# Performance work log

Measured on AMD Instinct MI355X. Metric: run time of the kernel, lower is better.

Reference implementation:

```python
import jax, jax.numpy as jnp
import numpy as np

FACTOR = 5  # init arg 'factor'


def setup_inputs() -> dict:
    key = jax.random.key(0)
    ks = jax.random.split(key, 9)
    B, L, H, D = 32, 4096, 8, 64
    sh = (B, L, H, D)
    scale = 0.125  # 1/sqrt(D)
    return {
        "queries": jax.random.normal(ks[0], sh, jnp.float32),
        "keys": jax.random.normal(ks[1], sh, jnp.float32),
        "values": jax.random.normal(ks[2], sh, jnp.float32),
        "Wq": jax.random.normal(ks[3], (1, D), jnp.float32) * scale,
        "bq": jax.random.normal(ks[4], (1,), jnp.float32) * scale,
        "Wk": jax.random.normal(ks[5], (1, D), jnp.float32) * scale,
        "bk": jax.random.normal(ks[6], (1,), jnp.float32) * scale,
        "Wv": jax.random.normal(ks[7], (1, D), jnp.float32) * scale,
        "bv": jax.random.normal(ks[8], (1,), jnp.float32) * scale,
    }


def reference(queries, keys, values, Wq, bq, Wk, bk, Wv, bv):
    B, L_Q, H, D = queries.shape
    # transpose(2,1) + LazyLinear(1) + squeeze  ->  scalar series per (b, h, t)
    q = jnp.einsum('blhd,d->bhl', queries, Wq[0]) + bq[0]  # [B,H,L_Q]
    k = jnp.einsum('blhd,d->bhl', keys, Wk[0]) + bk[0]
    v = jnp.einsum('blhd,d->bhl', values, Wv[0]) + bv[0]
    # L_K == L_Q here: torch takes the last L_Q steps (identity in this config)
    k = k[:, :, -L_Q:]
    v = v[:, :, -L_Q:]
    # FFT cross-correlation scores (rfft with n=2L-1 -> L bins; irfft default -> 2L-2)
    n_fft = 2 * L_Q - 1
    Qf = jnp.fft.rfft(q, n_fft)
    Kf = jnp.conj(jnp.fft.rfft(k, n_fft))
    score = jnp.fft.irfft(Qf * Kf)[:, :, :L_Q] / L_Q  # [B,H,L_Q]
    kk = FACTOR * int(np.ceil(np.log(L_Q)))  # 45 for L_Q=4096
    weight, top_idx = jax.lax.top_k(score, kk)  # [B,H,kk]
    weight = jax.nn.softmax(weight, axis=-1)
    # torch: indices = L_Q - top_idx - 1; rolled-V row j is roll(v, j+1),
    # i.e. shift = L_Q - top_idx, so V_sel[b,h,d,t] = v[b,h,(t + top_idx[b,h,d]) % L_Q].
    t = jnp.arange(L_Q)
    gidx = (top_idx[..., None] + t[None, None, None, :]) % L_Q  # [B,H,kk,L_Q]
    V_sel = jnp.take_along_axis(v[:, :, None, :], gidx, axis=-1)  # [B,H,kk,L_Q]
    out = jnp.einsum('bhd,bhdl->bhl', weight, V_sel)  # [B,H,L_Q]
    return out[..., None]  # [B,H,L_Q,1]
```

## Files before the change

kernel.cpp:

```cpp
#include <hip/hip_runtime.h>
#include <math.h>
#include <float.h>

#define L_   4096
#define M_   8192
#define H_   8
#define D_   64
#define KK   45

#define WS_C   0
#define WS_D   4096
#define WS_TW  8192
#define WS_H1  16384
#define WS_H2  24576
#define WS_QKV 32768

typedef unsigned int u32_t;

__device__ __forceinline__ float2 cadd(float2 a, float2 b) { return make_float2(a.x + b.x, a.y + b.y); }
__device__ __forceinline__ float2 csub(float2 a, float2 b) { return make_float2(a.x - b.x, a.y - b.y); }
__device__ __forceinline__ float2 cmulf(float2 a, float2 b) {
  return make_float2(a.x * b.x - a.y * b.y, a.x * b.y + a.y * b.x);
}
__device__ __forceinline__ float2 cmulcf(float2 a, float2 b) {
  return make_float2(a.x * b.x + a.y * b.y, a.y * b.x - a.x * b.y);
}

__device__ __forceinline__ float2 twf(int e) {
  float s, c;
  __sincosf((float)e * -7.66990394e-4f, &s, &c);
  return make_float2(c, s);
}

#define R4DIF(BUF) { \
  const float2 a = BUF[i0], b = BUF[i0 + q], c = BUF[i0 + 2 * q], d = BUF[i0 + 3 * q]; \
  const float2 t0 = cadd(a, c), t1 = csub(a, c), t2 = cadd(b, d), t3 = csub(b, d); \
  BUF[i0]         = cadd(t0, t2); \
  BUF[i0 + q]     = cmulf(make_float2(t1.x + t3.y, t1.y - t3.x), w1); \
  BUF[i0 + 2 * q] = cmulf(csub(t0, t2), w2); \
  BUF[i0 + 3 * q] = cmulf(make_float2(t1.x - t3.y, t1.y + t3.x), w3); }

#define R4DIT(BUF) { \
  const float2 z0 = BUF[i0]; \
  const float2 z1 = cmulcf(BUF[i0 + q],     w1); \
  const float2 z2 = cmulcf(BUF[i0 + 2 * q], w2); \
  const float2 z3 = cmulcf(BUF[i0 + 3 * q], w3); \
  const float2 t0 = cadd(z0, z2), t1 = csub(z0, z2), t2 = cadd(z1, z3), u = csub(z1, z3); \
  BUF[i0]         = cadd(t0, t2); \
  BUF[i0 + q]     = make_float2(t1.x - u.y, t1.y + u.x); \
  BUF[i0 + 2 * q] = csub(t0, t2); \
  BUF[i0 + 3 * q] = make_float2(t1.x + u.y, t1.y - u.x); }

__device__ __forceinline__ void bfly4_dif(float2 x[4], float2 w1, float2 w2, float2 w3) {
  const float2 t0 = cadd(x[0], x[2]), t1 = csub(x[0], x[2]);
  const float2 t2 = cadd(x[1], x[3]), t3 = csub(x[1], x[3]);
  x[0] = cadd(t0, t2);
  x[1] = cmulf(make_float2(t1.x + t3.y, t1.y - t3.x), w1);
  x[2] = cmulf(csub(t0, t2), w2);
  x[3] = cmulf(make_float2(t1.x - t3.y, t1.y + t3.x), w3);
}
__device__ __forceinline__ void bfly4_dit(float2 x[4], float2 w1, float2 w2, float2 w3) {
  const float2 z0 = x[0];
  const float2 z1 = cmulcf(x[1], w1);
  const float2 z2 = cmulcf(x[2], w2);
  const float2 z3 = cmulcf(x[3], w3);
  const float2 t0 = cadd(z0, z2), t1 = csub(z0, z2), t2 = cadd(z1, z3), u = csub(z1, z3);
  x[0] = cadd(t0, t2);
  x[1] = make_float2(t1.x - u.y, t1.y + u.x);
  x[2] = csub(t0, t2);
  x[3] = make_float2(t1.x + u.y, t1.y - u.x);
}

__device__ __forceinline__ float4 midpair(float4 a, float4 h) {
  float2 u = make_float2(a.x + a.z, a.y + a.w);
  float2 v = make_float2(a.x - a.z, a.y - a.w);
  u = cmulf(u, make_float2(h.x, h.y));
  v = cmulf(v, make_float2(h.z, h.w));
  return make_float4(u.x + v.x, u.y + v.y, u.x - v.x, u.y - v.y);
}

static __device__ void fwd_stages2(float2* A, float2* B) {
  const int tid = threadIdx.x;
  #pragma unroll
  for (int s = 1; s < 6; ++s) {
    const int q = 2048 >> (2 * s);
    __syncthreads();
    #pragma unroll
    for (int r = 0; r < 2; ++r) {
      const int bid = tid + (r << 10);
      const int j   = bid & (q - 1);
      const int i0  = ((bid >> (11 - 2 * s)) << (13 - 2 * s)) + j;
      const float2 w1 = twf(j << (2 * s));
      const float2 w2 = cmulf(w1, w1);
      const float2 w3 = cmulf(w2, w1);
      R4DIF(A) R4DIF(B)
    }
  }
}
static __device__ void inv_stages2(float2* A, float2* B) {
  const int tid = threadIdx.x;
  #pragma unroll
  for (int s = 5; s >= 1; --s) {
    const int q = 2048 >> (2 * s);
    __syncthreads();
    #pragma unroll
    for (int r = 0; r < 2; ++r) {
      const int bid = tid + (r << 10);
      const int j   = bid & (q - 1);
      const int i0  = ((bid >> (11 - 2 * s)) << (13 - 2 * s)) + j;
      const float2 w1 = twf(j << (2 * s));
      const float2 w2 = cmulf(w1, w1);
      const float2 w3 = cmulf(w2, w1);
      R4DIT(A) R4DIT(B)
    }
  }
}
static __device__ void fwd_stages1(float2* A) {
  const int tid = threadIdx.x;
  #pragma unroll
  for (int s = 1; s < 6; ++s) {
    const int q = 2048 >> (2 * s);
    __syncthreads();
    #pragma unroll
    for (int r = 0; r < 2; ++r) {
      const int bid = tid + (r << 10);
      const int j   = bid & (q - 1);
      const int i0  = ((bid >> (11 - 2 * s)) << (13 - 2 * s)) + j;
      const float2 w1 = twf(j << (2 * s));
      const float2 w2 = cmulf(w1, w1);
      const float2 w3 = cmulf(w2, w1);
      R4DIF(A)
    }
  }
}
static __device__ void inv_stages1(float2* A) {
  const int tid = threadIdx.x;
  #pragma unroll
  for (int s = 5; s >= 1; --s) {
    const int q = 2048 >> (2 * s);
    __syncthreads();
    #pragma unroll
    for (int r = 0; r < 2; ++r) {
      const int bid = tid + (r << 10);
      const int j   = bid & (q - 1);
      const int i0  = ((bid >> (11 - 2 * s)) << (13 - 2 * s)) + j;
      const float2 w1 = twf(j << (2 * s));
      const float2 w2 = cmulf(w1, w1);
      const float2 w3 = cmulf(w2, w1);
      R4DIT(A)
    }
  }
}

template <int NT>
static __device__ void fft_dif_tab(float2* buf, const float2* __restrict__ tw) {
  const int tid = threadIdx.x;
  for (int s = 0; s < 6; ++s) {
    const int q = 2048 >> (2 * s);
    __syncthreads();
    for (int r = 0; r < 2048 / NT; ++r) {
      const int bid = tid + r * NT;
      const int j   = bid & (q - 1);
      const int i0  = ((bid >> (11 - 2 * s)) << (13 - 2 * s)) + j;
      const int e   = j << (2 * s);
      const float2 w1 = tw[e], w2 = tw[2 * e], w3 = tw[3 * e];
      R4DIF(buf)
    }
  }
  __syncthreads();
  for (int r = 0; r < 4096 / NT; ++r) {
    const int i0 = (tid + r * NT) << 1;
    const float2 a = buf[i0], b = buf[i0 + 1];
    buf[i0] = cadd(a, b); buf[i0 + 1] = csub(a, b);
  }
  __syncthreads();
}

extern "C" __global__ void setup_tables(float2* ws) {
  const int idx = blockIdx.x * 512 + threadIdx.x;
  if (idx < 4096) {
    const long p = ((long)idx * idx) % 16382;
    const double th = -M_PI * (double)p / 8191.0;
    double s, c; sincos(th, &s, &c);
    ws[WS_C + idx] = make_float2((float)c, (float)s);
  } else if (idx < 8192) {
    const int j = idx - 4096;
    const long p = ((long)j * j) % 16380;
    const double th = M_PI * (double)p / 8190.0;
    double s, c; sincos(th, &s, &c);
    ws[WS_D + j] = make_float2((float)c, (float)s);
  } else if (idx < 16384) {
    const int j = idx - 8192;
    const double th = -M_PI * (double)j / 4096.0;
    double s, c; sincos(th, &s, &c);
    ws[WS_TW + j] = make_float2((float)c, (float)s);
  }
}

extern "C" __global__ __launch_bounds__(512, 1) void setup_filters(float2* ws) {
  __shared__ __align__(16) float2 buf[M_];
  const float2* src = ws + (blockIdx.x == 0 ? WS_C : WS_D);
  float2*       dst = ws + (blockIdx.x == 0 ? WS_H1 : WS_H2);
  const float2* tw  = ws + WS_TW;
  for (int i = threadIdx.x; i < M_; i += 512) {
    float2 val = make_float2(0.f, 0.f);
    if (i != 4096) {
      const int jj = (i <= 4095) ? i : (M_ - i);
      const float2 e = src[jj];
      val = make_float2(e.x, -e.y);
    }
    buf[i] = val;
  }
  fft_dif_tab<512>(buf, tw);
  const float sc = 1.0f / 8192.0f;
  for (int i = threadIdx.x; i < M_; i += 512)
    dst[i] = make_float2(buf[i].x * sc, buf[i].y * sc);
}

__device__ __forceinline__ void gll16(const float* gsrc, float* ldsbase) {
  __builtin_amdgcn_global_load_lds(
      (const __attribute__((address_space(1))) u32_t*)gsrc,
      (__attribute__((address_space(3))) u32_t*)ldsbase, 16, 0, 0);
}

extern "C" __global__ __launch_bounds__(256)
void proj_kernel(const float* __restrict__ queries, const float* __restrict__ keys,
                 const float* __restrict__ values,
                 const float* __restrict__ Wq, const float* __restrict__ bq,
                 const float* __restrict__ Wk, const float* __restrict__ bk,
                 const float* __restrict__ Wv, const float* __restrict__ bv,
                 float* __restrict__ q_ws, float* __restrict__ k_ws,
                 float* __restrict__ v_ws)
{
  __shared__ __align__(16) float lds[4][2][1024];

  const int tid  = threadIdx.x;
  const int w    = tid >> 6;
  const int lane = tid & 63;
  const int q16  = lane & 15;
  const int hi   = lane >> 4;
  const int blk  = blockIdx.x;
  const int b    = blk >> 6;
  const int b8   = b * 8;
  const int lbase = (blk & 63) << 6;

  const float* bases[3] = { queries + (size_t)b * 2097152,
                            keys    + (size_t)b * 2097152,
                            values  + (size_t)b * 2097152 };
  float* dsts[3] = { q_ws, k_ws, v_ws };
  const float4 wv4[3] = { reinterpret_cast<const float4*>(Wq)[q16],
                          reinterpret_cast<const float4*>(Wk)[q16],
                          reinterpret_cast<const float4*>(Wv)[q16] };
  const float bias3[3] = { bq[0], bk[0], bv[0] };

#define PR_SRC(IT) (bases[(IT) >> 3] + (size_t)(lbase + ((((IT) & 7) << 2) + w) * 2) * 512)
#define PR_ISSUE(IT) { \
    const float* g_ = PR_SRC(IT); \
    float* l_ = lds[w][(IT) & 1]; \
    gll16(g_ + 0 * 256 + lane * 4, l_ + 0 * 256); \
    gll16(g_ + 1 * 256 + lane * 4, l_ + 1 * 256); \
    gll16(g_ + 2 * 256 + lane * 4, l_ + 2 * 256); \
    gll16(g_ + 3 * 256 + lane * 4, l_ + 3 * 256); }

  PR_ISSUE(0)
  #pragma unroll
  for (int it = 0; it < 24; ++it) {
    if (it + 1 < 24) { PR_ISSUE(it + 1) }
    if (it == 0)           { asm volatile("s_waitcnt vmcnt(4)" ::: "memory"); }
    else if (it + 1 < 24)  { asm volatile("s_waitcnt vmcnt(8)" ::: "memory"); }
    else                   { asm volatile("s_waitcnt vmcnt(4)" ::: "memory"); }
    const int s_ = it >> 3;
    const float* L = lds[w][it & 1];
    const float4 wq_ = wv4[s_];
    float dj[4];
    #pragma unroll
    for (int j = 0; j < 4; ++j) {
      const float4 x = *reinterpret_cast<const float4*>(L + j * 256 + lane * 4);
      dj[j] = x.x * wq_.x + x.y * wq_.y + x.z * wq_.z + x.w * wq_.w;
    }
    #pragma unroll
    for (int j = 0; j < 4; ++j) {
      dj[j] += __shfl_xor(dj[j], 1);
      dj[j] += __shfl_xor(dj[j], 2);
      dj[j] += __shfl_xor(dj[j], 4);
      dj[j] += __shfl_xor(dj[j], 8);
    }
    if (q16 == 0) {
      const int l0 = lbase + (((it & 7) << 2) + w) * 2;
      float* dst = dsts[s_];
      const float bias = bias3[s_];
      #pragma unroll
      for (int j = 0; j < 4; ++j) {
        const int h = ((j & 1) << 2) + hi;
        dst[((size_t)(b8 + h) << 12) + l0 + (j >> 1)] = dj[j] + bias;
      }
    }
  }
#undef PR_ISSUE
#undef PR_SRC
}

extern "C" __global__ __launch_bounds__(1024, 1)
void autocorr_main(const float2* __restrict__ ws,
                   const float* __restrict__ q_ws, const float* __restrict__ k_ws,
                   const float* __restrict__ v_ws, float* __restrict__ outp)
{
  __shared__ __align__(16) float2 bufA[M_];
  __shared__ __align__(16) float2 bufB[M_];
  __shared__ float  v_lds[L_];
  __shared__ float  cand_v[16 * KK];
  __shared__ int    cand_i[16 * KK];
  __shared__ float  w_sh[KK];
  __shared__ int    i_sh[KK];

  const int tid = threadIdx.x;
  const int bh  = blockIdx.x;

  const float2* c_t = ws + WS_C;
  const float2* d_t = ws + WS_D;
  const float2* H1  = ws + WS_H1;
  const float2* H2  = ws + WS_H2;
  const float* qrow = q_ws + ((size_t)bh << 12);
  const float* krow = k_ws + ((size_t)bh << 12);
  const float* vrow = v_ws + ((size_t)bh << 12);

  {
    const float4 v4 = reinterpret_cast<const float4*>(vrow)[tid];
    reinterpret_cast<float4*>(v_lds)[tid] = v4;
  }

  #pragma unroll
  for (int r = 0; r < 2; ++r) {
    const int bid = tid + (r << 10);
    const float2 w1 = twf(bid);
    const float2 w2 = cmulf(w1, w1);
    const float2 w3 = cmulf(w2, w1);
    const float2 cc0 = c_t[bid], cc1 = c_t[bid + 2048];
    const float k0 = krow[bid], k1 = krow[bid + 2048];
    const float q0 = qrow[bid], q1 = qrow[bid + 2048];
    float2 xa[4] = { make_float2(k0 * cc0.x, k0 * cc0.y),
                     make_float2(k1 * cc1.x, k1 * cc1.y),
                     make_float2(0.f, 0.f), make_float2(0.f, 0.f) };
    float2 xb[4] = { make_float2(q0 * cc0.x, q0 * cc0.y),
                     make_float2(q1 * cc1.x, q1 * cc1.y),
                     make_float2(0.f, 0.f), make_float2(0.f, 0.f) };
    bfly4_dif(xa, w1, w2, w3);
    bfly4_dif(xb, w1, w2, w3);
    #pragma unroll
    for (int k = 0; k < 4; ++k) {
      bufA[bid + k * 2048] = xa[k];
      bufB[bid + k * 2048] = xb[k];
    }
  }

  fwd_stages2(bufA, bufB);
  __syncthreads();
  #pragma unroll
  for (int r = 0; r < 4; ++r) {
    const int p = tid + (r << 10);
    const float4 h = reinterpret_cast<const float4*>(H1)[p];
    reinterpret_cast<float4*>(bufA)[p] = midpair(reinterpret_cast<float4*>(bufA)[p], h);
    reinterpret_cast<float4*>(bufB)[p] = midpair(reinterpret_cast<float4*>(bufB)[p], h);
  }
  inv_stages2(bufA, bufB);
  __syncthreads();

  {
    float2 gd[2][2];
    #pragma unroll
    for (int r = 0; r < 2; ++r) {
      const int bid = tid + (r << 10);
      const float2 w1 = twf(bid);
      const float2 w2 = cmulf(w1, w1);
      const float2 w3 = cmulf(w2, w1);
      float2 xa[4], xb[4];
      #pragma unroll
      for (int k = 0; k < 4; ++k) { xa[k] = bufA[bid + k * 2048]; xb[k] = bufB[bid + k * 2048]; }
      bfly4_dit(xa, w1, w2, w3);
      bfly4_dit(xb, w1, w2, w3);
      #pragma unroll
      for (int k = 0; k < 2; ++k) {
        const int m = bid + k * 2048;
        const float2 cc = c_t[m];
        const float2 K = cmulf(cc, xa[k]);
        const float2 Q = cmulf(cc, xb[k]);
        const float2 F = cmulcf(Q, K);
        float2 g;
        if (m == 0 || m == 4095) g = make_float2(F.x, 0.f);
        else                     g = make_float2(2.f * F.x, 2.f * F.y);
        gd[r][k] = cmulf(g, d_t[m]);
      }
    }
    #pragma unroll
    for (int r = 0; r < 2; ++r) {
      const int bid = tid + (r << 10);
      const float2 w1 = twf(bid);
      const float2 w2 = cmulf(w1, w1);
      const float2 w3 = cmulf(w2, w1);
      float2 x[4] = { gd[r][0], gd[r][1], make_float2(0.f, 0.f), make_float2(0.f, 0.f) };
      bfly4_dif(x, w1, w2, w3);
      #pragma unroll
      for (int k = 0; k < 4; ++k) bufA[bid + k * 2048] = x[k];
    }
  }

  fwd_stages1(bufA);
  __syncthreads();
  #pragma unroll
  for (int r = 0; r < 4; ++r) {
    const int p = tid + (r << 10);
    const float4 h = reinterpret_cast<const float4*>(H2)[p];
    reinterpret_cast<float4*>(bufA)[p] = midpair(reinterpret_cast<float4*>(bufA)[p], h);
  }
  inv_stages1(bufA);
  __syncthreads();

  const float SCALE = (float)(1.0 / (8190.0 * 4096.0));
  float svv[4]; int sii[4];
  #pragma unroll
  for (int r = 0; r < 2; ++r) {
    const int bid = tid + (r << 10);
    const float2 w1 = twf(bid);
    const float2 w2 = cmulf(w1, w1);
    const float2 w3 = cmulf(w2, w1);
    float2 x[4];
    #pragma unroll
    for (int k = 0; k < 4; ++k) x[k] = bufA[bid + k * 2048];
    bfly4_dit(x, w1, w2, w3);
    #pragma unroll
    for (int k = 0; k < 2; ++k) {
      const int t = bid + k * 2048;
      const float2 Z = cmulf(d_t[t], x[k]);
      svv[2 * r + k] = Z.x * SCALE;
      sii[2 * r + k] = t;
    }
  }

  const int lane = tid & 63, wv = tid >> 6;
  for (int it = 0; it < KK; ++it) {
    float bvv = -FLT_MAX; int bii = 0x7fffffff;
    #pragma unroll
    for (int c = 0; c < 4; ++c)
      if (svv[c] > bvv || (svv[c] == bvv && sii[c] < bii)) { bvv = svv[c]; bii = sii[c]; }
    #pragma unroll
    for (int off = 1; off < 64; off <<= 1) {
      const float ov = __shfl_xor(bvv, off);
      const int   oi = __shfl_xor(bii, off);
      if (ov > bvv || (ov == bvv && oi < bii)) { bvv = ov; bii = oi; }
    }
    #pragma unroll
    for (int c = 0; c < 4; ++c) if (sii[c] == bii) svv[c] = -FLT_MAX;
    if (lane == 0) { cand_v[wv * KK + it] = bvv; cand_i[wv * KK + it] = bii; }
  }
  __syncthreads();

  if (tid < 64) {
    float mv[12]; int mi[12];
    #pragma unroll
    for (int c = 0; c < 12; ++c) {
      const int id = tid + 64 * c;
      if (id < 16 * KK) { mv[c] = cand_v[id]; mi[c] = cand_i[id]; }
      else              { mv[c] = -FLT_MAX;   mi[c] = 0x7fffffff; }
    }
    float m0 = 0.f, sum = 0.f, myv = -FLT_MAX; int myi = 0;
    for (int it = 0; it < KK; ++it) {
      float bvv = -FLT_MAX; int bii = 0x7fffffff;
      #pragma unroll
      for (int c = 0; c < 12; ++c)
        if (mv[c] > bvv || (mv[c] == bvv && mi[c] < bii)) { bvv = mv[c]; bii = mi[c]; }
      #pragma unroll
      for (int off = 1; off < 64; off <<= 1) {
        const float ov = __shfl_xor(bvv, off);
        const int   oi = __shfl_xor(bii, off);
        if (ov > bvv || (ov == bvv && oi < bii)) { bvv = ov; bii = oi; }
      }
      if (it == 0) m0 = bvv;
      sum += expf(bvv - m0);
      if (tid == it) { myv = bvv; myi = bii; }
      #pragma unroll
      for (int c = 0; c < 12; ++c) if (mi[c] == bii) mv[c] = -FLT_MAX;
    }
    if (tid < KK) { w_sh[tid] = expf(myv - m0) / sum; i_sh[tid] = myi; }
  }
  __syncthreads();

  {
    float acc[4] = {0, 0, 0, 0};
    for (int j = 0; j < KK; ++j) {
      const float wj = w_sh[j];
      const int   bse = i_sh[j] + tid;
      #pragma unroll
      for (int r = 0; r < 4; ++r)
        acc[r] = fmaf(wj, v_lds[(bse + (r << 10)) & (L_ - 1)], acc[r]);
    }
    float* op = outp + ((size_t)bh << 12);
    #pragma unroll
    for (int r = 0; r < 4; ++r) op[tid + (r << 10)] = acc[r];
  }
}

extern "C" void kernel_launch(void* const* d_in, const int* in_sizes, int n_in,
                              void* d_out, int out_size, void* d_ws, size_t ws_size,
                              hipStream_t stream) {
  const float* queries = (const float*)d_in[0];
  const float* keys    = (const float*)d_in[1];
  const float* values  = (const float*)d_in[2];
  const float* Wq = (const float*)d_in[3];
  const float* bq = (const float*)d_in[4];
  const float* Wk = (const float*)d_in[5];
  const float* bk = (const float*)d_in[6];
  const float* Wv = (const float*)d_in[7];
  const float* bv = (const float*)d_in[8];
  float2* ws = (float2*)d_ws;
  float* q_ws = (float*)d_ws + 2 * WS_QKV;
  float* k_ws = q_ws + (1 << 20);
  float* v_ws = k_ws + (1 << 20);
  float* out = (float*)d_out;

  hipLaunchKernelGGL(setup_tables,  dim3(32), dim3(512), 0, stream, ws);
  hipLaunchKernelGGL(setup_filters, dim3(2),  dim3(512), 0, stream, ws);
  hipLaunchKernelGGL(proj_kernel,   dim3(2048), dim3(256), 0, stream,
                     queries, keys, values, Wq, bq, Wk, bk, Wv, bv, q_ws, k_ws, v_ws);
  hipLaunchKernelGGL(autocorr_main, dim3(256), dim3(1024), 0, stream,
                     ws, q_ws, k_ws, v_ws, out);
}
```

Baseline: 330.8 us.

## Restructure projection kernel: per-tensor blocks, triple buffering, coalesced LDS-staged stores

The projection kernel now gives each block one tensor (q, k or v) and 256 rows of one batch, instead of all three tensors over 64 rows. Global-to-LDS loads are triple-buffered with three tiles in flight rather than two, to keep more memory traffic outstanding. Dot products are gathered in shared memory and written out as coalesced float4 stores, replacing the scattered scalar stores. The grid shrinks from 2048 to 1536 blocks and each block uses more LDS, which may lower occupancy.

```diff
diff --git a/kernel.cpp b/kernel.cpp
--- a/kernel.cpp
+++ b/kernel.cpp
@@ -232,7 +232,8 @@
                  float* __restrict__ q_ws, float* __restrict__ k_ws,
                  float* __restrict__ v_ws)
 {
-  __shared__ __align__(16) float lds[4][2][1024];
+  __shared__ __align__(16) float lds[4][3][1024];
+  __shared__ float dots_sh[8][256];
 
   const int tid  = threadIdx.x;
   const int w    = tid >> 6;
@@ -240,38 +241,37 @@
   const int q16  = lane & 15;
   const int hi   = lane >> 4;
   const int blk  = blockIdx.x;
-  const int b    = blk >> 6;
+  const int s    = blk >> 9;
+  const int rem  = blk & 511;
+  const int b    = rem >> 4;
+  const int rc   = rem & 15;
+  const int r0   = rc << 8;
   const int b8   = b * 8;
-  const int lbase = (blk & 63) << 6;
-
-  const float* bases[3] = { queries + (size_t)b * 2097152,
-                            keys    + (size_t)b * 2097152,
-                            values  + (size_t)b * 2097152 };
-  float* dsts[3] = { q_ws, k_ws, v_ws };
-  const float4 wv4[3] = { reinterpret_cast<const float4*>(Wq)[q16],
-                          reinterpret_cast<const float4*>(Wk)[q16],
-                          reinterpret_cast<const float4*>(Wv)[q16] };
-  const float bias3[3] = { bq[0], bk[0], bv[0] };
-
-#define PR_SRC(IT) (bases[(IT) >> 3] + (size_t)(lbase + ((((IT) & 7) << 2) + w) * 2) * 512)
+
+  const float* base = (s == 0 ? queries : (s == 1 ? keys : values))
+                      + (size_t)b * 2097152 + (size_t)r0 * 512;
+  const float4* W4p = reinterpret_cast<const float4*>(s == 0 ? Wq : (s == 1 ? Wk : Wv));
+  const float4 wq_ = W4p[q16];
+  const float bias = (s == 0 ? bq[0] : (s == 1 ? bk[0] : bv[0]));
+
+#define PR_SRC(IT) (base + (size_t)((((IT) << 2) + w) << 1) * 512)
 #define PR_ISSUE(IT) { \
     const float* g_ = PR_SRC(IT); \
-    float* l_ = lds[w][(IT) & 1]; \
+    float* l_ = lds[w][(IT) % 3]; \
     gll16(g_ + 0 * 256 + lane * 4, l_ + 0 * 256); \
     gll16(g_ + 1 * 256 + lane * 4, l_ + 1 * 256); \
     gll16(g_ + 2 * 256 + lane * 4, l_ + 2 * 256); \
     gll16(g_ + 3 * 256 + lane * 4, l_ + 3 * 256); }
 
   PR_ISSUE(0)
-  #pragma unroll
-  for (int it = 0; it < 24; ++it) {
-    if (it + 1 < 24) { PR_ISSUE(it + 1) }
-    if (it == 0)           { asm volatile("s_waitcnt vmcnt(4)" ::: "memory"); }
-    else if (it + 1 < 24)  { asm volatile("s_waitcnt vmcnt(8)" ::: "memory"); }
-    else                   { asm volatile("s_waitcnt vmcnt(4)" ::: "memory"); }
-    const int s_ = it >> 3;
-    const float* L = lds[w][it & 1];
-    const float4 wq_ = wv4[s_];
+  PR_ISSUE(1)
+  PR_ISSUE(2)
+  #pragma unroll
+  for (int it = 0; it < 32; ++it) {
+    if (it <= 29)      { asm volatile("s_waitcnt vmcnt(8)" ::: "memory"); }
+    else if (it == 30) { asm volatile("s_waitcnt vmcnt(4)" ::: "memory"); }
+    else               { asm volatile("s_waitcnt vmcnt(0)" ::: "memory"); }
+    const float* L = lds[w][it % 3];
     float dj[4];
     #pragma unroll
     for (int j = 0; j < 4; ++j) {
@@ -286,18 +286,34 @@
       dj[j] += __shfl_xor(dj[j], 8);
     }
     if (q16 == 0) {
-      const int l0 = lbase + (((it & 7) << 2) + w) * 2;
-      float* dst = dsts[s_];
-      const float bias = bias3[s_];
+      const int rl = (((it << 2) + w) << 1);
       #pragma unroll
       for (int j = 0; j < 4; ++j) {
         const int h = ((j & 1) << 2) + hi;
-        dst[((size_t)(b8 + h) << 12) + l0 + (j >> 1)] = dj[j] + bias;
+        dots_sh[h][rl + (j >> 1)] = dj[j];
       }
     }
+    if (it + 3 < 32) { PR_ISSUE(it + 3) }
   }
 #undef PR_ISSUE
 #undef PR_SRC
+
+  __syncthreads();
+  {
+    float* dst = (s == 0 ? q_ws : (s == 1 ? k_ws : v_ws));
+    #pragma unroll
+    for (int p = 0; p < 2; ++p) {
+      const int fl4 = tid + (p << 8);
+      const int h   = fl4 >> 6;
+      const int i64 = fl4 & 63;
+      float4 o;
+      o.x = dots_sh[h][i64 * 4 + 0] + bias;
+      o.y = dots_sh[h][i64 * 4 + 1] + bias;
+      o.z = dots_sh[h][i64 * 4 + 2] + bias;
+      o.w = dots_sh[h][i64 * 4 + 3] + bias;
+      reinterpret_cast<float4*>(dst + ((size_t)(b8 + h) << 12) + r0)[i64] = o;
+    }
+  }
 }
 
 extern "C" __global__ __launch_bounds__(1024, 1)
@@ -519,7 +535,7 @@
 
   hipLaunchKernelGGL(setup_tables,  dim3(32), dim3(512), 0, stream, ws);
   hipLaunchKernelGGL(setup_filters, dim3(2),  dim3(512), 0, stream, ws);
-  hipLaunchKernelGGL(proj_kernel,   dim3(2048), dim3(256), 0, stream,
+  hipLaunchKernelGGL(proj_kernel,   dim3(1536), dim3(256), 0, stream,
                      queries, keys, values, Wq, bq, Wk, bk, Wv, bv, q_ws, k_ws, v_ws);
   hipLaunchKernelGGL(autocorr_main, dim3(256), dim3(1024), 0, stream,
                      ws, q_ws, k_ws, v_ws, out);
```

Result: faster. 314.8 us (-4.8%).
